# Kernel optimization log

Hardware: AMD Instinct MI355X
Metric: run time of the kernel (lower is better)

## Reference

```python
import jax, jax.numpy as jnp
import numpy as np

B, T, H, E = 256, 256, 512, 96  # batch, enc seq len, hidden/enc dim, charset size


def setup_inputs() -> dict:
    key = jax.random.key(0)
    ks = jax.random.split(key, 9)
    s = 0.05  # param scale
    return {
        "prev_h": jax.random.normal(ks[0], (B, H), jnp.float32),
        "prev_c": jax.random.normal(ks[1], (B, H), jnp.float32),
        "batch_H": jax.random.normal(ks[2], (B, T, H), jnp.float32),
        "char_onehots": jax.nn.one_hot(jax.random.randint(ks[3], (B,), 0, E), E, dtype=jnp.float32),
        "W_i2h": jax.random.normal(ks[4], (H, H), jnp.float32) * s,
        "W_h2h": jax.random.normal(ks[5], (H, H), jnp.float32) * s,
        "b_h2h": jnp.zeros((H,), jnp.float32),
        "w_score": jax.random.normal(ks[6], (H, 1), jnp.float32) * s,
        "W_lstm": jax.random.normal(ks[7], (H + E, 4 * H), jnp.float32) * s,
        "U_lstm": jax.random.normal(ks[8], (H, 4 * H), jnp.float32) * s,
        "b_lstm": jnp.zeros((4 * H,), jnp.float32),
    }


def reference(prev_h, prev_c, batch_H, char_onehots,
              W_i2h, W_h2h, b_h2h, w_score, W_lstm, U_lstm, b_lstm):
    # Additive (Bahdanau) attention
    proj = jnp.einsum('btd,dh->bth', batch_H, W_i2h)          # [B,T,H]
    hp = prev_h @ W_h2h + b_h2h                               # [B,H]
    e = jnp.tanh(proj + hp[:, None, :]) @ w_score             # [B,T,1]
    alpha = jax.nn.softmax(e, axis=1)                         # [B,T,1]
    context = jnp.einsum('bt,btd->bd', alpha[..., 0], batch_H)  # [B,D]
    x = jnp.concatenate([context, char_onehots], axis=1)      # [B,D+E]
    # Keras LSTMCell: gate order i, f, c(g), o
    z = x @ W_lstm + prev_h @ U_lstm + b_lstm                 # [B,4H]
    i, f, g, o = jnp.split(z, 4, axis=1)
    c_new = jax.nn.sigmoid(f) * prev_c + jax.nn.sigmoid(i) * jnp.tanh(g)
    h_new = jax.nn.sigmoid(o) * jnp.tanh(c_new)
    return h_new, c_new, alpha
```

## Files before the change

kernel.cpp:

```cpp
#include <hip/hip_runtime.h>
#include <hip/hip_bf16.h>
#include <math.h>

#define Bq 256
#define Tq 256
#define Hq 512
#define Eq 96

typedef __attribute__((ext_vector_type(8))) short short8;
typedef __attribute__((ext_vector_type(4))) float f32x4;

static __device__ __forceinline__ unsigned short f2bf(float f) {
  union { float f; unsigned u; } v; v.f = f;
  unsigned r = v.u + 0x7FFF + ((v.u >> 16) & 1);
  return (unsigned short)(r >> 16);
}

static __device__ __forceinline__ float sat_tanh(float x) {
  float ax = fminf(fabsf(x), 15.0f);
  float e = __builtin_exp2f(ax * 2.885390082f);
  float t = 1.0f - 2.0f / (e + 1.0f);
  return copysignf(t, x);
}

static __device__ __forceinline__ float sat_sig(float x) {
  float cx = fmaxf(fminf(x, 30.0f), -30.0f);
  return 1.0f / (1.0f + __builtin_exp2f(-cx * 1.442695041f));
}

__global__ __launch_bounds__(256) void convW_k(const float* __restrict__ W,
                                               unsigned short* __restrict__ Wt) {
  __shared__ float tile[32][33];
  int bx = blockIdx.x & 15, by = blockIdx.x >> 4;
  int tx = threadIdx.x & 31, ty = threadIdx.x >> 5;
  #pragma unroll
  for (int i = 0; i < 32; i += 8)
    tile[ty + i][tx] = W[(size_t)(by * 32 + ty + i) * Hq + bx * 32 + tx];
  __syncthreads();
  #pragma unroll
  for (int i = 0; i < 32; i += 8)
    Wt[(size_t)(bx * 32 + ty + i) * Hq + by * 32 + tx] = f2bf(tile[tx][ty + i]);
}

__global__ __launch_bounds__(256) void hsplit_k(const float* __restrict__ ph,
                                                const float* __restrict__ Whh,
                                                float* __restrict__ hp) {
  __shared__ __align__(16) float xs[8][128];
  const int ks = blockIdx.x & 3;
  const int nc = (blockIdx.x >> 2) & 3;
  const int bg = blockIdx.x >> 4;
  const int tid = threadIdx.x;
  const int row0 = bg * 8;
  const int d0 = ks * 128;
  for (int i = tid; i < 8 * 32; i += 256) {
    int r = i >> 5, dd = (i & 31) * 4;
    *(float4*)&xs[r][dd] = *(const float4*)&ph[(size_t)(row0 + r) * Hq + d0 + dd];
  }
  __syncthreads();
  const int rt = tid >> 6;
  const int ct = tid & 63;
  const int n = nc * 128 + ct * 2;
  float a00 = 0, a01 = 0, a10 = 0, a11 = 0;
  for (int dd = 0; dd < 128; dd += 4) {
    float4 x0 = *(const float4*)&xs[rt * 2][dd];
    float4 x1 = *(const float4*)&xs[rt * 2 + 1][dd];
    #pragma unroll
    for (int j = 0; j < 4; j++) {
      float2 w = *(const float2*)&Whh[(size_t)(d0 + dd + j) * Hq + n];
      float xj0 = ((const float*)&x0)[j];
      float xj1 = ((const float*)&x1)[j];
      a00 += xj0 * w.x; a01 += xj0 * w.y;
      a10 += xj1 * w.x; a11 += xj1 * w.y;
    }
  }
  int row = row0 + rt * 2;
  atomicAdd(&hp[(size_t)row * Hq + n], a00);
  atomicAdd(&hp[(size_t)row * Hq + n + 1], a01);
  atomicAdd(&hp[(size_t)(row + 1) * Hq + n], a10);
  atomicAdd(&hp[(size_t)(row + 1) * Hq + n + 1], a11);
}

#define BM 128
#define BN 128
#define BK 32
#define LDK 40

__global__ __launch_bounds__(256) void fused_score_k(
    const float* __restrict__ A,
    const unsigned short* __restrict__ Wt,
    const float* __restrict__ hp,
    const float* __restrict__ bh,
    const float* __restrict__ wsc,
    float* __restrict__ e) {
  __shared__ unsigned short As[BM * LDK];
  __shared__ unsigned short Bs[BN * LDK];
  __shared__ float hps[BN];
  __shared__ float wss[BN];

  const int tid = threadIdx.x;
  const int m0 = blockIdx.x * BM;
  const int n0 = blockIdx.y * BN;
  const int bb = m0 >> 8;

  if (tid < BN) {
    hps[tid] = hp[(size_t)bb * Hq + n0 + tid] + bh[n0 + tid];
    wss[tid] = wsc[n0 + tid];
  }

  const int wave = tid >> 6;
  const int lane = tid & 63;
  const int quad = lane >> 4;
  const int l16 = lane & 15;
  const int wm = (wave & 1) * 64;
  const int wn = (wave >> 1) * 64;

  f32x4 acc[4][4] = {};

  const int arow = tid >> 3;
  const int acol = (tid & 7) * 4;
  const int brow = tid >> 2;
  const int bkh = (tid & 3) * 8;

  for (int k0 = 0; k0 < Hq; k0 += BK) {
    __syncthreads();
    #pragma unroll
    for (int p = 0; p < 4; p++) {
      int r = arow + p * 32;
      const float4 v = *(const float4*)(&A[(size_t)(m0 + r) * Hq + k0 + acol]);
      ushort4 pk;
      pk.x = f2bf(v.x); pk.y = f2bf(v.y); pk.z = f2bf(v.z); pk.w = f2bf(v.w);
      *(ushort4*)&As[r * LDK + acol] = pk;
    }
    #pragma unroll
    for (int p = 0; p < 2; p++) {
      int r = brow + p * 64;
      const uint4 v = *(const uint4*)(&Wt[(size_t)(n0 + r) * Hq + k0 + bkh]);
      *(uint4*)&Bs[r * LDK + bkh] = v;
    }
    __syncthreads();

    short8 af[4], bfr[4];
    #pragma unroll
    for (int mi = 0; mi < 4; mi++)
      af[mi] = *(const short8*)&As[(wm + mi * 16 + l16) * LDK + quad * 8];
    #pragma unroll
    for (int ni = 0; ni < 4; ni++)
      bfr[ni] = *(const short8*)&Bs[(wn + ni * 16 + l16) * LDK + quad * 8];
    #pragma unroll
    for (int mi = 0; mi < 4; mi++)
      #pragma unroll
      for (int ni = 0; ni < 4; ni++)
        acc[mi][ni] = __builtin_amdgcn_mfma_f32_16x16x32_bf16(
            af[mi], bfr[ni], acc[mi][ni], 0, 0, 0);
  }

  float hv[4], wv[4];
  #pragma unroll
  for (int ni = 0; ni < 4; ni++) {
    int c = wn + ni * 16 + l16;
    hv[ni] = hps[c];
    wv[ni] = wss[c];
  }
  #pragma unroll
  for (int mi = 0; mi < 4; mi++) {
    float s[4] = {0, 0, 0, 0};
    #pragma unroll
    for (int ni = 0; ni < 4; ni++)
      #pragma unroll
      for (int r = 0; r < 4; r++)
        s[r] += sat_tanh(acc[mi][ni][r] + hv[ni]) * wv[ni];
    #pragma unroll
    for (int r = 0; r < 4; r++) {
      s[r] += __shfl_xor(s[r], 8, 64);
      s[r] += __shfl_xor(s[r], 4, 64);
      s[r] += __shfl_xor(s[r], 2, 64);
      s[r] += __shfl_xor(s[r], 1, 64);
    }
    if (l16 == 0) {
      int row = m0 + wm + mi * 16 + quad * 4;
      #pragma unroll
      for (int r = 0; r < 4; r++) atomicAdd(&e[row + r], s[r]);
    }
  }
}

__global__ __launch_bounds__(256) void softmax_k(float* __restrict__ ea) {
  __shared__ float red[8];
  int b = blockIdx.x, t = threadIdx.x;
  int wave = t >> 6, lane = t & 63;
  float x = ea[b * Tq + t];
  float m = x;
  #pragma unroll
  for (int off = 32; off >= 1; off >>= 1) m = fmaxf(m, __shfl_xor(m, off, 64));
  if (lane == 0) red[wave] = m;
  __syncthreads();
  m = fmaxf(fmaxf(red[0], red[1]), fmaxf(red[2], red[3]));
  float ex = __builtin_exp2f((x - m) * 1.442695041f);
  float s = ex;
  #pragma unroll
  for (int off = 32; off >= 1; off >>= 1) s += __shfl_xor(s, off, 64);
  if (lane == 0) red[4 + wave] = s;
  __syncthreads();
  s = red[4] + red[5] + red[6] + red[7];
  ea[b * Tq + t] = ex / s;
}

__global__ __launch_bounds__(256) void ctxsplit_k(const float* __restrict__ alpha,
                                                  const float* __restrict__ bH,
                                                  float* __restrict__ ctx) {
  __shared__ float al[64];
  const int b = blockIdx.x >> 2;
  const int tc = blockIdx.x & 3;
  const int tid = threadIdx.x;
  if (tid < 64) al[tid] = alpha[b * Tq + tc * 64 + tid];
  __syncthreads();
  const float2* Hp = (const float2*)(bH + (size_t)b * Tq * Hq + (size_t)tc * 64 * Hq);
  float ax = 0.f, ay = 0.f;
  #pragma unroll 8
  for (int t = 0; t < 64; t++) {
    float a = al[t];
    float2 v = Hp[t * (Hq / 2) + tid];
    ax += a * v.x;
    ay += a * v.y;
  }
  atomicAdd(&ctx[(size_t)b * Hq + 2 * tid], ax);
  atomicAdd(&ctx[(size_t)b * Hq + 2 * tid + 1], ay);
}

__global__ __launch_bounds__(256) void zsplit_k(
    const float* __restrict__ ctx, const float* __restrict__ oneh,
    const float* __restrict__ ph, const float* __restrict__ Wl,
    const float* __restrict__ Ul, float* __restrict__ z) {
  __shared__ __align__(16) float xs[8 * 280];
  const int ks = blockIdx.x & 3;
  const int hc = (blockIdx.x >> 2) & 7;
  const int bg = blockIdx.x >> 5;
  const int tid = threadIdx.x;
  const int row0 = bg * 8;
  const int dbase = ks * 280;

  for (int i = tid; i < 8 * 280; i += 256) {
    int r = i / 280, dd = i % 280;
    int g = dbase + dd;
    float v;
    if (g < 512) v = ctx[(size_t)(row0 + r) * Hq + g];
    else if (g < 608) v = oneh[(row0 + r) * Eq + (g - 512)];
    else v = ph[(size_t)(row0 + r) * Hq + (g - 608)];
    xs[r * 280 + dd] = v;
  }
  __syncthreads();

  const int rt = tid >> 6;
  const int ct = tid & 63;
  const int c0 = ct * 4;
  const int gate = c0 >> 6;
  const int ho = c0 & 63;
  const int n = gate * 512 + hc * 64 + ho;

  float acc0[4] = {0, 0, 0, 0};
  float acc1[4] = {0, 0, 0, 0};
  const float* xr0 = &xs[(rt * 2) * 280];
  const float* xr1 = &xs[(rt * 2 + 1) * 280];

  for (int dd = 0; dd < 280; dd += 4) {
    float4 x0 = *(const float4*)&xr0[dd];
    float4 x1 = *(const float4*)&xr1[dd];
    #pragma unroll
    for (int j = 0; j < 4; j++) {
      int d = dbase + dd + j;
      const float* wp = (d < 608) ? &Wl[(size_t)d * 2048 + n]
                                  : &Ul[(size_t)(d - 608) * 2048 + n];
      float4 w = *(const float4*)wp;
      float a = ((const float*)&x0)[j], b = ((const float*)&x1)[j];
      acc0[0] += a * w.x; acc0[1] += a * w.y; acc0[2] += a * w.z; acc0[3] += a * w.w;
      acc1[0] += b * w.x; acc1[1] += b * w.y; acc1[2] += b * w.z; acc1[3] += b * w.w;
    }
  }
  const int r0 = row0 + rt * 2;
  #pragma unroll
  for (int j = 0; j < 4; j++) {
    atomicAdd(&z[(size_t)r0 * 2048 + n + j], acc0[j]);
    atomicAdd(&z[(size_t)(r0 + 1) * 2048 + n + j], acc1[j]);
  }
}

__global__ __launch_bounds__(256) void gatesz_k(const float* __restrict__ z,
                                                const float* __restrict__ bl,
                                                const float* __restrict__ pc,
                                                float* __restrict__ outh,
                                                float* __restrict__ outc) {
  int p = blockIdx.x * 256 + threadIdx.x;
  #pragma unroll
  for (int q = 0; q < 2; q++, p += 65536) {
    int r = p >> 9, h = p & 511;
    const float* zb = z + (size_t)r * 2048;
    float gi = zb[h] + bl[h];
    float gf = zb[512 + h] + bl[512 + h];
    float gg = zb[1024 + h] + bl[1024 + h];
    float go = zb[1536 + h] + bl[1536 + h];
    float cn = sat_sig(gf) * pc[p] + sat_sig(gi) * sat_tanh(gg);
    float hn = sat_sig(go) * sat_tanh(cn);
    outh[p] = hn;
    outc[p] = cn;
  }
}

#define KXc 1120
__global__ __launch_bounds__(256) void zgates2_k(
    const float* __restrict__ ctx, const float* __restrict__ oneh,
    const float* __restrict__ ph, const float* __restrict__ pc,
    const float* __restrict__ Wl, const float* __restrict__ Ul,
    const float* __restrict__ bl,
    float* __restrict__ outh, float* __restrict__ outc) {
  __shared__ __align__(16) float xs[8 * KXc];
  const int bg = blockIdx.x >> 3;
  const int hc = blockIdx.x & 7;
  const int tid = threadIdx.x;
  const int row0 = bg * 8;

  for (int i = tid; i < 8 * 128; i += 256) {
    int r = i >> 7, dd = (i & 127) * 4;
    *(float4*)&xs[r * KXc + dd] = *(const float4*)&ctx[(size_t)(row0 + r) * Hq + dd];
  }
  for (int i = tid; i < 8 * 128; i += 256) {
    int r = i >> 7, dd = (i & 127) * 4;
    *(float4*)&xs[r * KXc + 608 + dd] = *(const float4*)&ph[(size_t)(row0 + r) * Hq + dd];
  }
  if (tid < 8 * 24) {
    int r = tid / 24, dd = (tid % 24) * 4;
    *(float4*)&xs[r * KXc + 512 + dd] = *(const float4*)&oneh[(row0 + r) * Eq + dd];
  }
  __syncthreads();

  const int rt = tid >> 6;
  const int ct = tid & 63;
  const int c0 = ct * 4;
  const int gate = c0 >> 6;
  const int ho = c0 & 63;
  const int n = gate * 512 + hc * 64 + ho;

  float acc0[4] = {0, 0, 0, 0};
  float acc1[4] = {0, 0, 0, 0};
  const float* xr0 = &xs[(rt * 2) * KXc];
  const float* xr1 = &xs[(rt * 2 + 1) * KXc];

  for (int d = 0; d < 608; d += 4) {
    float4 x0 = *(const float4*)&xr0[d];
    float4 x1 = *(const float4*)&xr1[d];
    #pragma unroll
    for (int j = 0; j < 4; j++) {
      float4 w = *(const float4*)&Wl[(size_t)(d + j) * 2048 + n];
      float a = ((const float*)&x0)[j], b = ((const float*)&x1)[j];
      acc0[0] += a * w.x; acc0[1] += a * w.y; acc0[2] += a * w.z; acc0[3] += a * w.w;
      acc1[0] += b * w.x; acc1[1] += b * w.y; acc1[2] += b * w.z; acc1[3] += b * w.w;
    }
  }
  for (int d = 0; d < 512; d += 4) {
    float4 x0 = *(const float4*)&xr0[608 + d];
    float4 x1 = *(const float4*)&xr1[608 + d];
    #pragma unroll
    for (int j = 0; j < 4; j++) {
      float4 w = *(const float4*)&Ul[(size_t)(d + j) * 2048 + n];
      float a = ((const float*)&x0)[j], b = ((const float*)&x1)[j];
      acc0[0] += a * w.x; acc0[1] += a * w.y; acc0[2] += a * w.z; acc0[3] += a * w.w;
      acc1[0] += b * w.x; acc1[1] += b * w.y; acc1[2] += b * w.z; acc1[3] += b * w.w;
    }
  }

  __syncthreads();
  float* zs = xs;
  #pragma unroll
  for (int j = 0; j < 4; j++) {
    zs[(rt * 2) * 256 + c0 + j] = acc0[j];
    zs[(rt * 2 + 1) * 256 + c0 + j] = acc1[j];
  }
  __syncthreads();

  #pragma unroll
  for (int p = tid; p < 512; p += 256) {
    int r = p >> 6, o = p & 63;
    int h = hc * 64 + o;
    int grow = row0 + r;
    float gi = zs[r * 256 + o]       + bl[h];
    float gf = zs[r * 256 + 64 + o]  + bl[512 + h];
    float gg = zs[r * 256 + 128 + o] + bl[1024 + h];
    float go = zs[r * 256 + 192 + o] + bl[1536 + h];
    float cn = sat_sig(gf) * pc[(size_t)grow * Hq + h] + sat_sig(gi) * sat_tanh(gg);
    float hn = sat_sig(go) * sat_tanh(cn);
    outh[(size_t)grow * Hq + h] = hn;
    outc[(size_t)grow * Hq + h] = cn;
  }
}

extern "C" void kernel_launch(void* const* d_in, const int* in_sizes, int n_in,
                              void* d_out, int out_size, void* d_ws, size_t ws_size,
                              hipStream_t stream) {
  const float* prev_h = (const float*)d_in[0];
  const float* prev_c = (const float*)d_in[1];
  const float* batch_H = (const float*)d_in[2];
  const float* oneh = (const float*)d_in[3];
  const float* W_i2h = (const float*)d_in[4];
  const float* W_h2h = (const float*)d_in[5];
  const float* b_h2h = (const float*)d_in[6];
  const float* w_score = (const float*)d_in[7];
  const float* W_lstm = (const float*)d_in[8];
  const float* U_lstm = (const float*)d_in[9];
  const float* b_lstm = (const float*)d_in[10];

  float* out = (float*)d_out;
  float* outh = out;
  float* outc = out + Bq * Hq;
  float* alpha = out + 2 * Bq * Hq;

  float* ws = (float*)d_ws;
  float* hp = ws;
  float* ctx = ws;
  unsigned short* Wt = (unsigned short*)(ws + 131072);
  float* z = ws + 131072;

  const bool bigws = ws_size >= 2621440;

  hipMemsetAsync(alpha, 0, Bq * Tq * sizeof(float), stream);
  hipMemsetAsync(hp, 0, Bq * Hq * sizeof(float), stream);
  convW_k<<<256, 256, 0, stream>>>(W_i2h, Wt);
  hsplit_k<<<512, 256, 0, stream>>>(prev_h, W_h2h, hp);
  dim3 g2(512, 4);
  fused_score_k<<<g2, 256, 0, stream>>>(batch_H, Wt, hp, b_h2h, w_score, alpha);
  softmax_k<<<256, 256, 0, stream>>>(alpha);
  if (bigws) {
    hipMemsetAsync(ws, 0, 2621440, stream);
    ctxsplit_k<<<1024, 256, 0, stream>>>(alpha, batch_H, ctx);
    zsplit_k<<<1024, 256, 0, stream>>>(ctx, oneh, prev_h, W_lstm, U_lstm, z);
    gatesz_k<<<256, 256, 0, stream>>>(z, b_lstm, prev_c, outh, outc);
  } else {
    hipMemsetAsync(ctx, 0, Bq * Hq * sizeof(float), stream);
    ctxsplit_k<<<1024, 256, 0, stream>>>(alpha, batch_H, ctx);
    zgates2_k<<<256, 256, 0, stream>>>(ctx, oneh, prev_h, prev_c,
                                       W_lstm, U_lstm, b_lstm, outh, outc);
  }
}
```

Before: 399.4 us.

## Restructure score GEMM: full-N per block, B from global, double-buffered A

The fused attention-score kernel now gives each block 64 rows and all 512 columns, with each wave covering 128 columns. B fragments are read directly from global memory (the bf16 W^T, L2-resident) instead of being staged in LDS. A tiles are double-buffered in LDS with register prefetch of the next tile, and a single barrier per step replaces the previous two. Because each block sees every column, the row scores are reduced in LDS and written directly, which removes the atomics and the alpha memset. The trade-off is more accumulator registers (128 floats per lane) and repeated global reads of B by every block.

```diff
diff --git a/kernel.cpp b/kernel.cpp
--- a/kernel.cpp
+++ b/kernel.cpp
@@ -14,6 +14,12 @@
   union { float f; unsigned u; } v; v.f = f;
   unsigned r = v.u + 0x7FFF + ((v.u >> 16) & 1);
   return (unsigned short)(r >> 16);
+}
+
+static __device__ __forceinline__ ushort4 pack4(float4 v) {
+  ushort4 p;
+  p.x = f2bf(v.x); p.y = f2bf(v.y); p.z = f2bf(v.z); p.w = f2bf(v.w);
+  return p;
 }
 
 static __device__ __forceinline__ float sat_tanh(float x) {
@@ -80,92 +86,88 @@
   atomicAdd(&hp[(size_t)(row + 1) * Hq + n + 1], a11);
 }
 
-#define BM 128
-#define BN 128
-#define BK 32
 #define LDK 40
 
-__global__ __launch_bounds__(256) void fused_score_k(
+__global__ __launch_bounds__(256, 2) void fused_score_k(
     const float* __restrict__ A,
     const unsigned short* __restrict__ Wt,
     const float* __restrict__ hp,
     const float* __restrict__ bh,
     const float* __restrict__ wsc,
     float* __restrict__ e) {
-  __shared__ unsigned short As[BM * LDK];
-  __shared__ unsigned short Bs[BN * LDK];
-  __shared__ float hps[BN];
-  __shared__ float wss[BN];
+  __shared__ unsigned short As[2][64 * LDK];
+  __shared__ float red[4][64];
 
   const int tid = threadIdx.x;
-  const int m0 = blockIdx.x * BM;
-  const int n0 = blockIdx.y * BN;
-  const int bb = m0 >> 8;
-
-  if (tid < BN) {
-    hps[tid] = hp[(size_t)bb * Hq + n0 + tid] + bh[n0 + tid];
-    wss[tid] = wsc[n0 + tid];
-  }
-
+  const int m0 = blockIdx.x * 64;
+  const int b = m0 >> 8;
   const int wave = tid >> 6;
   const int lane = tid & 63;
   const int quad = lane >> 4;
   const int l16 = lane & 15;
-  const int wm = (wave & 1) * 64;
-  const int wn = (wave >> 1) * 64;
-
-  f32x4 acc[4][4] = {};
+  const int wn = wave * 128;
 
   const int arow = tid >> 3;
   const int acol = (tid & 7) * 4;
-  const int brow = tid >> 2;
-  const int bkh = (tid & 3) * 8;
-
-  for (int k0 = 0; k0 < Hq; k0 += BK) {
-    __syncthreads();
-    #pragma unroll
-    for (int p = 0; p < 4; p++) {
-      int r = arow + p * 32;
-      const float4 v = *(const float4*)(&A[(size_t)(m0 + r) * Hq + k0 + acol]);
-      ushort4 pk;
-      pk.x = f2bf(v.x); pk.y = f2bf(v.y); pk.z = f2bf(v.z); pk.w = f2bf(v.w);
-      *(ushort4*)&As[r * LDK + acol] = pk;
-    }
-    #pragma unroll
-    for (int p = 0; p < 2; p++) {
-      int r = brow + p * 64;
-      const uint4 v = *(const uint4*)(&Wt[(size_t)(n0 + r) * Hq + k0 + bkh]);
-      *(uint4*)&Bs[r * LDK + bkh] = v;
-    }
-    __syncthreads();
-
-    short8 af[4], bfr[4];
+  const float* Ab = A + (size_t)m0 * Hq;
+  const unsigned short* Bp = Wt + (size_t)(wn + l16) * Hq + quad * 8;
+
+  f32x4 acc[4][8] = {};
+
+  {
+    float4 v0 = *(const float4*)&Ab[(size_t)arow * Hq + acol];
+    float4 v1 = *(const float4*)&Ab[(size_t)(arow + 32) * Hq + acol];
+    *(ushort4*)&As[0][arow * LDK + acol] = pack4(v0);
+    *(ushort4*)&As[0][(arow + 32) * LDK + acol] = pack4(v1);
+  }
+  __syncthreads();
+
+  for (int step = 0; step < 16; step++) {
+    const int k0 = step * 32;
+    const int cur = step & 1;
+
+    float4 n0v, n1v;
+    if (step < 15) {
+      n0v = *(const float4*)&Ab[(size_t)arow * Hq + k0 + 32 + acol];
+      n1v = *(const float4*)&Ab[(size_t)(arow + 32) * Hq + k0 + 32 + acol];
+    }
+
+    short8 bfr[8];
+    #pragma unroll
+    for (int ni = 0; ni < 8; ni++)
+      bfr[ni] = *(const short8*)(Bp + (size_t)ni * 16 * Hq + k0);
+
+    short8 af[4];
     #pragma unroll
     for (int mi = 0; mi < 4; mi++)
-      af[mi] = *(const short8*)&As[(wm + mi * 16 + l16) * LDK + quad * 8];
-    #pragma unroll
-    for (int ni = 0; ni < 4; ni++)
-      bfr[ni] = *(const short8*)&Bs[(wn + ni * 16 + l16) * LDK + quad * 8];
+      af[mi] = *(const short8*)&As[cur][(mi * 16 + l16) * LDK + quad * 8];
+
     #pragma unroll
     for (int mi = 0; mi < 4; mi++)
       #pragma unroll
-      for (int ni = 0; ni < 4; ni++)
+      for (int ni = 0; ni < 8; ni++)
         acc[mi][ni] = __builtin_amdgcn_mfma_f32_16x16x32_bf16(
             af[mi], bfr[ni], acc[mi][ni], 0, 0, 0);
-  }
-
-  float hv[4], wv[4];
-  #pragma unroll
-  for (int ni = 0; ni < 4; ni++) {
+
+    if (step < 15) {
+      *(ushort4*)&As[cur ^ 1][arow * LDK + acol] = pack4(n0v);
+      *(ushort4*)&As[cur ^ 1][(arow + 32) * LDK + acol] = pack4(n1v);
+    }
+    __syncthreads();
+  }
+
+  float hv[8], wv[8];
+  #pragma unroll
+  for (int ni = 0; ni < 8; ni++) {
     int c = wn + ni * 16 + l16;
-    hv[ni] = hps[c];
-    wv[ni] = wss[c];
+    hv[ni] = hp[(size_t)b * Hq + c] + bh[c];
+    wv[ni] = wsc[c];
   }
   #pragma unroll
   for (int mi = 0; mi < 4; mi++) {
     float s[4] = {0, 0, 0, 0};
     #pragma unroll
-    for (int ni = 0; ni < 4; ni++)
+    for (int ni = 0; ni < 8; ni++)
       #pragma unroll
       for (int r = 0; r < 4; r++)
         s[r] += sat_tanh(acc[mi][ni][r] + hv[ni]) * wv[ni];
@@ -177,11 +179,13 @@
       s[r] += __shfl_xor(s[r], 1, 64);
     }
     if (l16 == 0) {
-      int row = m0 + wm + mi * 16 + quad * 4;
       #pragma unroll
-      for (int r = 0; r < 4; r++) atomicAdd(&e[row + r], s[r]);
-    }
-  }
+      for (int r = 0; r < 4; r++) red[wave][mi * 16 + quad * 4 + r] = s[r];
+    }
+  }
+  __syncthreads();
+  if (tid < 64)
+    e[m0 + tid] = red[0][tid] + red[1][tid] + red[2][tid] + red[3][tid];
 }
 
 __global__ __launch_bounds__(256) void softmax_k(float* __restrict__ ea) {
@@ -420,12 +424,10 @@
 
   const bool bigws = ws_size >= 2621440;
 
-  hipMemsetAsync(alpha, 0, Bq * Tq * sizeof(float), stream);
   hipMemsetAsync(hp, 0, Bq * Hq * sizeof(float), stream);
   convW_k<<<256, 256, 0, stream>>>(W_i2h, Wt);
   hsplit_k<<<512, 256, 0, stream>>>(prev_h, W_h2h, hp);
-  dim3 g2(512, 4);
-  fused_score_k<<<g2, 256, 0, stream>>>(batch_H, Wt, hp, b_h2h, w_score, alpha);
+  fused_score_k<<<1024, 256, 0, stream>>>(batch_H, Wt, hp, b_h2h, w_score, alpha);
   softmax_k<<<256, 256, 0, stream>>>(alpha);
   if (bigws) {
     hipMemsetAsync(ws, 0, 2621440, stream);
```

Measured after the change: 399.2 us. Within noise of the previous version (-0.0%).
